# Optimization experiments

Hardware: AMD Instinct MI355X
Metric: run time of the kernel (lower is better)

Reference implementation:

```python
import jax, jax.numpy as jnp
import numpy as np

B, L, D = 16, 1024, 1024
H = 8
K = D // H
OUT = 64

def setup_inputs() -> dict:
    key = jax.random.key(0)
    ks = jax.random.split(key, 12)
    std = 0.1
    return {
        "x0": jax.random.normal(ks[0], (B, L, D), jnp.float32),
        "x1": jax.random.normal(ks[1], (B, L, D), jnp.float32),
        "x2": jax.random.normal(ks[2], (B, L, D), jnp.float32),
        "support": jax.random.normal(ks[3], (B, L), jnp.float32),
        "mask": jnp.ones((B, L), jnp.float32),
        "Wk": std * jax.random.normal(ks[4], (D, D), jnp.float32),   # tokeys.weight
        "Wq": std * jax.random.normal(ks[5], (D, D), jnp.float32),   # toqueries.weight
        "Wv": std * jax.random.normal(ks[6], (D, D), jnp.float32),   # tovalues.weight
        "Wu": std * jax.random.normal(ks[7], (D, D), jnp.float32),   # unifyheads.weight
        "bu": std * jax.random.normal(ks[8], (D,), jnp.float32),     # unifyheads.bias
        "Wmlp": std * jax.random.normal(ks[9], (OUT, D), jnp.float32),
        "bmlp": std * jax.random.normal(ks[10], (OUT,), jnp.float32),
    }

def reference(x0, x1, x2, support, mask, Wk, Wq, Wv, Wu, bu, Wmlp, bmlp):
    # SelfAttention with first=True: q from x2 via tokeys, k from x1 via toqueries, v from x0 via tovalues
    b, l, d = x0.shape
    h, k = H, K
    scale = k ** (-0.25)  # applied to both q and k, as in the torch code
    q = (x2 @ Wk.T).reshape(b, l, h, k) * scale
    key_ = (x1 @ Wq.T).reshape(b, l, h, k) * scale
    v = (x0 @ Wv.T).reshape(b, l, h, k)
    dot = jnp.einsum('blhk,bmhk->bhlm', q, key_)          # [b,h,l,l]
    attn = jax.nn.softmax(dot, axis=-1)
    out = jnp.einsum('bhlm,bmhk->blhk', attn, v).reshape(b, l, d)
    out = out @ Wu.T + bu                                  # unifyheads
    pooled = jnp.mean(out, axis=1) + jnp.max(out, axis=1)  # 'mean_and_max'
    logits = pooled @ Wmlp.T + bmlp                        # dropout = identity (eval)
    return logits
```

## Files before the change

kernel.cpp:

```cpp
#include <hip/hip_runtime.h>

using u16 = unsigned short;
using u32 = unsigned int;
using short8 = __attribute__((ext_vector_type(8))) short;
using floatx4 = __attribute__((ext_vector_type(4))) float;
using floatx16 = __attribute__((ext_vector_type(16))) float;
using u32x4 = __attribute__((ext_vector_type(4))) u32;

__device__ __forceinline__ u32 fbits(float f) { union { float f; u32 u; } v; v.f = f; return v.u; }
__device__ __forceinline__ float fofb(u32 u) { union { u32 u; float f; } v; v.u = u; return v.f; }

__device__ __forceinline__ u16 f2bf(float f) {
    u32 u = fbits(f);
    return (u16)((u + 0x7FFFu + ((u >> 16) & 1u)) >> 16);
}

__device__ __forceinline__ u32 cvtpk_bf16(float lo, float hi) {
    u32 r;
    asm("v_cvt_pk_bf16_f32 %0, %1, %2" : "=v"(r) : "v"(lo), "v"(hi));
    return r;
}

__device__ __forceinline__ void cvt_split8(const float* x, short8& h, short8& l) {
#pragma unroll
    for (int j = 0; j < 8; ++j) {
        u32 b = fbits(x[j]);
        h[j] = (short)(b >> 16);
        float r = x[j] - fofb(b & 0xffff0000u);
        l[j] = (short)(fbits(r) >> 16);
    }
}
__device__ __forceinline__ void cvt_rne8(const float* x, short8& h) {
#pragma unroll
    for (int j = 0; j < 8; ++j) h[j] = (short)f2bf(x[j]);
}

__device__ __forceinline__ void load_lds16(const void* g, u16* l) {
    __builtin_amdgcn_global_load_lds(
        (const __attribute__((address_space(1))) unsigned int*)(g),
        (__attribute__((address_space(3))) unsigned int*)(l), 16, 0, 0);
}

__global__ void convw_kernel(const float* __restrict__ W0, const float* __restrict__ W1,
                             const float* __restrict__ W2, const float* __restrict__ W3,
                             u16* __restrict__ D0, u16* __restrict__ D1,
                             u16* __restrict__ D2, u16* __restrict__ D3) {
    int y = blockIdx.y;
    const float* s = (y == 0) ? W0 : (y == 1) ? W1 : (y == 2) ? W2 : W3;
    u16* d = (y == 0) ? D0 : (y == 1) ? D1 : (y == 2) ? D2 : D3;
    int i = (blockIdx.x * 256 + threadIdx.x) * 4;
    float4 v = *reinterpret_cast<const float4*>(s + i);
    ushort4 h;
    h.x = f2bf(v.x); h.y = f2bf(v.y); h.z = f2bf(v.z); h.w = f2bf(v.w);
    *reinterpret_cast<ushort4*>(d + i) = h;
}

#define GK 1024
#define GN 1024

template<bool SPLIT, bool TRANS, bool POOL, bool FP32A>
__global__ __launch_bounds__(256)
void gemm_bt(const void* __restrict__ Av, const u16* __restrict__ Bh,
             u16* __restrict__ Cb, float scale, u16* __restrict__ Vt,
             float* __restrict__ psum, float* __restrict__ pmax)
{
    constexpr int SM = TRANS ? 17408 : (FP32A ? 12288 : 8192);
    __shared__ __align__(16) u16 smem[SM];

    const int tid  = threadIdx.x;
    const int lane = tid & 63, wave = tid >> 6;
    const int quad = lane >> 4, l15 = lane & 15;
    const int wr = wave >> 1, wc = wave & 1;
    const int bm = blockIdx.x * 128, bn = blockIdx.y * 128;

    const int BOff = FP32A ? 8192 : 4096;

    floatx4 acc[4][4];
#pragma unroll
    for (int mt = 0; mt < 4; ++mt)
#pragma unroll
        for (int nt = 0; nt < 4; ++nt)
#pragma unroll
            for (int r = 0; r < 4; ++r) acc[mt][nt][r] = 0.f;

    const int s8 = (quad ^ ((l15 >> 1) & 3)) * 8;

    for (int kt = 0; kt < GK; kt += 32) {
        __syncthreads();
        if (FP32A) {
            const float* Af = (const float*)Av;
            const int arow = lane >> 3, achk = (lane & 7) ^ (lane >> 3);
            const int brow = lane >> 2, bchk = (lane & 3) ^ ((lane >> 3) & 3);
#pragma unroll
            for (int j = 0; j < 6; ++j) {
                int n = wave + 4 * j;
                if (n < 16) {
                    load_lds16(Af + (size_t)(bm + n * 8 + arow) * GK + kt + achk * 4,
                               smem + n * 512);
                } else {
                    int m = n - 16;
                    load_lds16(Bh + (size_t)(bn + m * 16 + brow) * GK + kt + bchk * 8,
                               smem + 8192 + m * 512);
                }
            }
        } else {
            const u16* Ab = (const u16*)Av;
            const int cgl = (lane & 3) ^ ((lane >> 3) & 3);
            const int rl  = lane >> 2;
            const u16* gp = (wave < 2) ? Ab : Bh;
            int rowb = (wave < 2) ? bm : bn;
            u16* lp = smem + (wave >> 1) * 4096;
            int q0 = (wave & 1) * 4;
#pragma unroll
            for (int q = 0; q < 4; ++q) {
                int qq = q0 + q;
                load_lds16(gp + (size_t)(rowb + qq * 16 + rl) * GK + cgl * 8 + kt,
                           lp + qq * 512);
            }
        }
        __syncthreads();

        short8 a_h[4], a_l[4], b_h[4];
        if (FP32A) {
            const float* Af4 = (const float*)smem;
#pragma unroll
            for (int mt = 0; mt < 4; ++mt) {
                int ra = wr * 64 + mt * 16 + l15;
                int f = ra & 7;
                float xv[8];
                *reinterpret_cast<float4*>(xv) =
                    *reinterpret_cast<const float4*>(Af4 + ra * 32 + (((2 * quad) ^ f) * 4));
                *reinterpret_cast<float4*>(xv + 4) =
                    *reinterpret_cast<const float4*>(Af4 + ra * 32 + (((2 * quad + 1) ^ f) * 4));
                if (SPLIT) cvt_split8(xv, a_h[mt], a_l[mt]);
                else       cvt_rne8(xv, a_h[mt]);
            }
        } else {
#pragma unroll
            for (int mt = 0; mt < 4; ++mt) {
                int ra = wr * 64 + mt * 16 + l15;
                a_h[mt] = *reinterpret_cast<const short8*>(smem + ra * 32 + s8);
            }
        }
#pragma unroll
        for (int nt = 0; nt < 4; ++nt) {
            int rb = wc * 64 + nt * 16 + l15;
            b_h[nt] = *reinterpret_cast<const short8*>(smem + BOff + rb * 32 + s8);
        }
#pragma unroll
        for (int mt = 0; mt < 4; ++mt)
#pragma unroll
            for (int nt = 0; nt < 4; ++nt)
                acc[mt][nt] = __builtin_amdgcn_mfma_f32_16x16x32_bf16(a_h[mt], b_h[nt], acc[mt][nt], 0, 0, 0);
        if (SPLIT) {
#pragma unroll
            for (int mt = 0; mt < 4; ++mt)
#pragma unroll
                for (int nt = 0; nt < 4; ++nt)
                    acc[mt][nt] = __builtin_amdgcn_mfma_f32_16x16x32_bf16(a_l[mt], b_h[nt], acc[mt][nt], 0, 0, 0);
        }
    }

    if (POOL) {
#pragma unroll
        for (int nt = 0; nt < 4; ++nt) {
            float s = 0.f, m = -3.0e38f;
#pragma unroll
            for (int mt = 0; mt < 4; ++mt)
#pragma unroll
                for (int r = 0; r < 4; ++r) {
                    float v = acc[mt][nt][r];
                    s += v; m = fmaxf(m, v);
                }
            s += __shfl_xor(s, 16); s += __shfl_xor(s, 32);
            m = fmaxf(m, __shfl_xor(m, 16)); m = fmaxf(m, __shfl_xor(m, 32));
            if (quad == 0) {
                int col = bn + wc * 64 + nt * 16 + l15;
                int chunk = (bm >> 6) + wr;
                psum[chunk * 1024 + col] = s;
                pmax[chunk * 1024 + col] = m;
            }
        }
    } else if (!TRANS) {
#pragma unroll
        for (int mt = 0; mt < 4; ++mt)
#pragma unroll
            for (int nt = 0; nt < 4; ++nt)
#pragma unroll
                for (int r = 0; r < 4; ++r) {
                    int row = bm + wr * 64 + mt * 16 + quad * 4 + r;
                    int col = bn + wc * 64 + nt * 16 + l15;
                    Cb[(size_t)row * GN + col] = f2bf(acc[mt][nt][r] * scale);
                }
    } else {
        __syncthreads();
#pragma unroll
        for (int mt = 0; mt < 4; ++mt)
#pragma unroll
            for (int nt = 0; nt < 4; ++nt)
#pragma unroll
                for (int r = 0; r < 4; ++r) {
                    int row_local = wr * 64 + mt * 16 + quad * 4 + r;
                    int col_local = wc * 64 + nt * 16 + l15;
                    smem[col_local * 136 + row_local] = f2bf(acc[mt][nt][r]);
                }
        __syncthreads();
        int b = bm >> 10, l0 = bm & 1023, h = bn >> 7;
        int d = tid >> 1, rblk = (tid & 1) * 64;
        u16* gv = Vt + ((size_t)(b * 8 + h) * 128 + d) * 1024 + l0 + rblk;
#pragma unroll
        for (int v = 0; v < 8; ++v)
            *reinterpret_cast<short8*>(gv + v * 8) =
                *reinterpret_cast<const short8*>(smem + d * 136 + rblk + v * 8);
    }
}

#define LOG2E 1.44269504088896f
#define EXPC  46.1662413084470f

__global__ __launch_bounds__(256, 2)
void attn_kernel(const u16* __restrict__ Q, const u16* __restrict__ Kk,
                 const u16* __restrict__ Vt, u16* __restrict__ AO)
{
    __shared__ __align__(16) u16 Ks[2][64 * 128];
    __shared__ __align__(16) u16 Vts[2][128 * 64];

    const int tid  = threadIdx.x;
    const int lane = tid & 63, wave = tid >> 6;
    const int l31 = lane & 31, h2 = lane >> 5;
    const int l7 = lane & 7;

    const int lin = blockIdx.x + (blockIdx.y << 3) + (blockIdx.z << 6);
    const int qt = lin >> 7;
    const int hd = lin & 7;
    const int b  = (lin >> 3) & 15;

    short8 qf[8];
    {
        int qrow = b * 1024 + qt * 128 + wave * 32 + l31;
        const u16* qp = Q + (size_t)qrow * 1024 + hd * 128 + h2 * 8;
#pragma unroll
        for (int s = 0; s < 8; ++s)
            qf[s] = *reinterpret_cast<const short8*>(qp + s * 16);
    }

    float lsum = 0.f;
    floatx16 oacc[4];
#pragma unroll
    for (int db = 0; db < 4; ++db)
#pragma unroll
        for (int r = 0; r < 16; ++r) oacc[db][r] = 0.f;

    const int krow_l = lane >> 4;
    const u16* kgB[4];
#pragma unroll
    for (int i = 0; i < 4; ++i) {
        int cg = (lane & 15) ^ ((i * 4 + krow_l) & 7);
        kgB[i] = Kk + (size_t)(b * 1024 + wave * 16 + i * 4 + krow_l) * 1024
                    + hd * 128 + cg * 8;
    }
    const u16* vtb = Vt + (size_t)(b * 8 + hd) * 128 * 1024;
    const int vrow_l = lane >> 3;
    const u16* vgB = vtb + (size_t)(wave * 32 + vrow_l) * 1024
                         + (((lane & 7) ^ vrow_l) * 8);

#pragma unroll
    for (int i = 0; i < 4; ++i)
        load_lds16(kgB[i], &Ks[0][(wave * 16 + i * 4) * 128]);
#pragma unroll
    for (int i = 0; i < 4; ++i)
        load_lds16(vgB + (size_t)i * 8 * 1024, &Vts[0][(wave * 32 + i * 8) * 64]);

    for (int t = 0; t < 16; ++t) {
        const int cur = t & 1;
        asm volatile("s_waitcnt vmcnt(0)" ::: "memory");
        __builtin_amdgcn_s_barrier();
        __builtin_amdgcn_sched_barrier(0);
        if (t < 15) {
            const int nxt = cur ^ 1;
#pragma unroll
            for (int i = 0; i < 4; ++i)
                load_lds16(kgB[i] + (size_t)(t + 1) * 64 * 1024,
                           &Ks[nxt][(wave * 16 + i * 4) * 128]);
#pragma unroll
            for (int i = 0; i < 4; ++i)
                load_lds16(vgB + (size_t)i * 8 * 1024 + (size_t)(t + 1) * 64,
                           &Vts[nxt][(wave * 32 + i * 8) * 64]);
        }
        const u16* ksb = Ks[cur];
        const u16* vsb = Vts[cur];

        short8 pfr[4];
#pragma unroll
        for (int kb = 0; kb < 2; ++kb) {
            floatx16 sacc;
#pragma unroll
            for (int r = 0; r < 16; ++r) sacc[r] = 0.f;
            __builtin_amdgcn_s_setprio(1);
#pragma unroll
            for (int s = 0; s < 8; ++s) {
                short8 kfr = *reinterpret_cast<const short8*>(
                    &ksb[(kb * 32 + l31) * 128 + (((s * 2 + h2) ^ l7) * 8)]);
                sacc = __builtin_amdgcn_mfma_f32_32x32x16_bf16(kfr, qf[s], sacc, 0, 0, 0);
            }
            __builtin_amdgcn_s_setprio(0);
#pragma unroll
            for (int r = 0; r < 16; ++r) {
                float p = exp2f(fmaf(sacc[r], LOG2E, -EXPC));
                sacc[r] = p;
                lsum += p;
            }
            u32 c0[4], c1[4];
#pragma unroll
            for (int qd = 0; qd < 4; ++qd) {
                c0[qd] = cvtpk_bf16(sacc[4 * qd + 0], sacc[4 * qd + 1]);
                c1[qd] = cvtpk_bf16(sacc[4 * qd + 2], sacc[4 * qd + 3]);
            }
#pragma unroll
            for (int pb = 0; pb < 2; ++pb) {
                auto r1a = __builtin_amdgcn_permlane32_swap(c0[2 * pb],     c1[2 * pb],     false, false);
                auto r2a = __builtin_amdgcn_permlane32_swap(c1[2 * pb],     c0[2 * pb],     false, false);
                auto r1b = __builtin_amdgcn_permlane32_swap(c0[2 * pb + 1], c1[2 * pb + 1], false, false);
                auto r2b = __builtin_amdgcn_permlane32_swap(c1[2 * pb + 1], c0[2 * pb + 1], false, false);
                u32 w0 = h2 ? (u32)r2b[0] : (u32)r1a[0];
                u32 w1 = h2 ? (u32)r1b[0] : (u32)r2a[0];
                u32 w2 = h2 ? (u32)r2b[1] : (u32)r1a[1];
                u32 w3 = h2 ? (u32)r1b[1] : (u32)r2a[1];
                u32x4 ww = {w0, w1, w2, w3};
                pfr[kb * 2 + pb] = __builtin_bit_cast(short8, ww);
            }
        }

        __builtin_amdgcn_s_setprio(1);
#pragma unroll
        for (int ks = 0; ks < 4; ++ks) {
#pragma unroll
            for (int db = 0; db < 4; ++db) {
                int d = db * 32 + l31;
                short8 vfr = *reinterpret_cast<const short8*>(
                    &vsb[d * 64 + (((ks * 2 + h2) ^ l7) * 8)]);
                oacc[db] = __builtin_amdgcn_mfma_f32_32x32x16_bf16(pfr[ks], vfr, oacc[db], 0, 0, 0);
            }
        }
        __builtin_amdgcn_s_setprio(0);
    }

    lsum += __shfl_xor(lsum, 32);

    int qbase = b * 1024 + qt * 128 + wave * 32;
#pragma unroll
    for (int rg = 0; rg < 4; ++rg)
#pragma unroll
        for (int r = 0; r < 4; ++r) {
            int row = rg * 8 + 4 * h2 + r;
            float inv = 1.0f / __shfl(lsum, row);
            u16* ao = AO + (size_t)(qbase + row) * 1024 + hd * 128 + l31;
#pragma unroll
            for (int db = 0; db < 4; ++db)
                ao[db * 32] = f2bf(oacc[db][rg * 4 + r] * inv);
        }
}

__global__ __launch_bounds__(256)
void head_kernel(const float* __restrict__ psum, const float* __restrict__ pmax,
                 const float* __restrict__ bu, const float* __restrict__ Wmlp,
                 const float* __restrict__ bmlp, float* __restrict__ out) {
    __shared__ float pool_s[1024];
    int b = blockIdx.x, tid = threadIdx.x;
    int c4 = tid * 4;
    float4 s = {0.f, 0.f, 0.f, 0.f};
    float4 m = {-3.0e38f, -3.0e38f, -3.0e38f, -3.0e38f};
#pragma unroll
    for (int c = 0; c < 16; ++c) {
        float4 a = *reinterpret_cast<const float4*>(psum + (size_t)(b * 16 + c) * 1024 + c4);
        float4 x = *reinterpret_cast<const float4*>(pmax + (size_t)(b * 16 + c) * 1024 + c4);
        s.x += a.x; s.y += a.y; s.z += a.z; s.w += a.w;
        m.x = fmaxf(m.x, x.x); m.y = fmaxf(m.y, x.y);
        m.z = fmaxf(m.z, x.z); m.w = fmaxf(m.w, x.w);
    }
    float4 bb = *reinterpret_cast<const float4*>(bu + c4);
    pool_s[c4 + 0] = s.x * (1.0f / 1024.0f) + m.x + 2.0f * bb.x;
    pool_s[c4 + 1] = s.y * (1.0f / 1024.0f) + m.y + 2.0f * bb.y;
    pool_s[c4 + 2] = s.z * (1.0f / 1024.0f) + m.z + 2.0f * bb.z;
    pool_s[c4 + 3] = s.w * (1.0f / 1024.0f) + m.w + 2.0f * bb.w;
    __syncthreads();
    int o = tid >> 2, seg = tid & 3;
    const float4* wr = reinterpret_cast<const float4*>(Wmlp + o * 1024 + seg * 256);
    const float4* pr = reinterpret_cast<const float4*>(pool_s + seg * 256);
    float acc = 0.f;
#pragma unroll 8
    for (int i = 0; i < 64; ++i) {
        float4 a = pr[i], w = wr[i];
        acc += a.x * w.x + a.y * w.y + a.z * w.z + a.w * w.w;
    }
    acc += __shfl_xor(acc, 1);
    acc += __shfl_xor(acc, 2);
    if (seg == 0) out[b * 64 + o] = acc + bmlp[o];
}

extern "C" void kernel_launch(void* const* d_in, const int* in_sizes, int n_in,
                              void* d_out, int out_size, void* d_ws, size_t ws_size,
                              hipStream_t stream) {
    const float* x0 = (const float*)d_in[0];
    const float* x1 = (const float*)d_in[1];
    const float* x2 = (const float*)d_in[2];
    const float* Wk = (const float*)d_in[5];
    const float* Wq = (const float*)d_in[6];
    const float* Wv = (const float*)d_in[7];
    const float* Wu = (const float*)d_in[8];
    const float* bu = (const float*)d_in[9];
    const float* Wmlp = (const float*)d_in[10];
    const float* bmlp = (const float*)d_in[11];
    float* out = (float*)d_out;

    char* ws = (char*)d_ws;
    const size_t MB32 = 33554432ull;
    size_t wo = 0;
    u16* Wkh = (u16*)(ws + wo); wo += 2097152;
    u16* Wqh = (u16*)(ws + wo); wo += 2097152;
    u16* Wvh = (u16*)(ws + wo); wo += 2097152;
    u16* Wuh = (u16*)(ws + wo); wo += 2097152;
    u16* Qb = (u16*)(ws + wo); wo += MB32;
    u16* Kb = (u16*)(ws + wo); wo += MB32;
    u16* Vt = (u16*)(ws + wo); wo += MB32;
    u16* AOb = (u16*)(ws + wo); wo += MB32;
    float* psum = (float*)(ws + wo); wo += 1048576;
    float* pmax = (float*)(ws + wo); wo += 1048576;
    if (ws_size < wo) return;

    const float scale = 0.29730177875068026f;

    convw_kernel<<<dim3(1024, 4), 256, 0, stream>>>(Wk, Wq, Wv, Wu, Wkh, Wqh, Wvh, Wuh);

    dim3 ggrid(128, 8);
    gemm_bt<true, false, false, true><<<ggrid, 256, 0, stream>>>(x2, Wkh, Qb, scale, nullptr, nullptr, nullptr);
    gemm_bt<true, false, false, true><<<ggrid, 256, 0, stream>>>(x1, Wqh, Kb, scale, nullptr, nullptr, nullptr);
    gemm_bt<false, true, false, true><<<ggrid, 256, 0, stream>>>(x0, Wvh, nullptr, 1.0f, Vt, nullptr, nullptr);

    dim3 agrid(8, 8, 16);
    attn_kernel<<<agrid, 256, 0, stream>>>(Qb, Kb, Vt, AOb);

    gemm_bt<false, false, true, false><<<ggrid, 256, 0, stream>>>(AOb, Wuh, nullptr, 1.0f, nullptr, psum, pmax);

    head_kernel<<<16, 256, 0, stream>>>(psum, pmax, bu, Wmlp, bmlp, out);
}
```

Measured before the change: 596.4 us.

## Pre-split fp32 activations into bf16 hi/lo and run K=2048 bf16 GEMMs

Adds a conversion pass that writes each fp32 input as concatenated bf16 hi and lo halves, and duplicates Wk/Wq along K. The Q/K projections then become plain bf16 GEMMs with K=2048 instead of fp32-A loads with in-kernel split conversion, and the V projection uses a pre-rounded bf16 input. The intent is to remove the fp32 LDS traffic and the per-tile conversion work inside the GEMM. The cost is three extra elementwise passes over 64MB inputs, extra workspace traffic, and a doubled K loop for two GEMMs.

```diff
diff --git a/kernel.cpp b/kernel.cpp
--- a/kernel.cpp
+++ b/kernel.cpp
@@ -41,6 +41,7 @@
         (__attribute__((address_space(3))) unsigned int*)(l), 16, 0, 0);
 }
 
+template<bool DUP>
 __global__ void convw_kernel(const float* __restrict__ W0, const float* __restrict__ W1,
                              const float* __restrict__ W2, const float* __restrict__ W3,
                              u16* __restrict__ D0, u16* __restrict__ D1,
@@ -52,13 +53,47 @@
     float4 v = *reinterpret_cast<const float4*>(s + i);
     ushort4 h;
     h.x = f2bf(v.x); h.y = f2bf(v.y); h.z = f2bf(v.z); h.w = f2bf(v.w);
-    *reinterpret_cast<ushort4*>(d + i) = h;
-}
-
-#define GK 1024
+    if (DUP && y < 2) {
+        int n = i >> 10, k = i & 1023;
+        u16* base = d + (size_t)n * 2048 + k;
+        *reinterpret_cast<ushort4*>(base) = h;
+        *reinterpret_cast<ushort4*>(base + 1024) = h;
+    } else {
+        *reinterpret_cast<ushort4*>(d + i) = h;
+    }
+}
+
+template<bool SPLIT>
+__global__ __launch_bounds__(256)
+void convx_kernel(const float* __restrict__ X, u16* __restrict__ O) {
+    int i = (blockIdx.x * 256 + threadIdx.x) * 4;
+    float4 v = *reinterpret_cast<const float4*>(X + i);
+    if (SPLIT) {
+        int m = i >> 10, k = i & 1023;
+        float xs[4] = {v.x, v.y, v.z, v.w};
+        ushort4 h, l;
+        u16 hh[4], ll[4];
+#pragma unroll
+        for (int j = 0; j < 4; ++j) {
+            u32 b = fbits(xs[j]);
+            hh[j] = (u16)(b >> 16);
+            float r = xs[j] - fofb(b & 0xffff0000u);
+            ll[j] = (u16)(fbits(r) >> 16);
+        }
+        h.x = hh[0]; h.y = hh[1]; h.z = hh[2]; h.w = hh[3];
+        l.x = ll[0]; l.y = ll[1]; l.z = ll[2]; l.w = ll[3];
+        *reinterpret_cast<ushort4*>(O + (size_t)m * 2048 + k) = h;
+        *reinterpret_cast<ushort4*>(O + (size_t)m * 2048 + 1024 + k) = l;
+    } else {
+        ushort4 h;
+        h.x = f2bf(v.x); h.y = f2bf(v.y); h.z = f2bf(v.z); h.w = f2bf(v.w);
+        *reinterpret_cast<ushort4*>(O + i) = h;
+    }
+}
+
 #define GN 1024
 
-template<bool SPLIT, bool TRANS, bool POOL, bool FP32A>
+template<int KDIM, bool SPLIT, bool TRANS, bool POOL, bool FP32A>
 __global__ __launch_bounds__(256)
 void gemm_bt(const void* __restrict__ Av, const u16* __restrict__ Bh,
              u16* __restrict__ Cb, float scale, u16* __restrict__ Vt,
@@ -85,7 +120,7 @@
 
     const int s8 = (quad ^ ((l15 >> 1) & 3)) * 8;
 
-    for (int kt = 0; kt < GK; kt += 32) {
+    for (int kt = 0; kt < KDIM; kt += 32) {
         __syncthreads();
         if (FP32A) {
             const float* Af = (const float*)Av;
@@ -95,11 +130,11 @@
             for (int j = 0; j < 6; ++j) {
                 int n = wave + 4 * j;
                 if (n < 16) {
-                    load_lds16(Af + (size_t)(bm + n * 8 + arow) * GK + kt + achk * 4,
+                    load_lds16(Af + (size_t)(bm + n * 8 + arow) * KDIM + kt + achk * 4,
                                smem + n * 512);
                 } else {
                     int m = n - 16;
-                    load_lds16(Bh + (size_t)(bn + m * 16 + brow) * GK + kt + bchk * 8,
+                    load_lds16(Bh + (size_t)(bn + m * 16 + brow) * KDIM + kt + bchk * 8,
                                smem + 8192 + m * 512);
                 }
             }
@@ -114,7 +149,7 @@
 #pragma unroll
             for (int q = 0; q < 4; ++q) {
                 int qq = q0 + q;
-                load_lds16(gp + (size_t)(rowb + qq * 16 + rl) * GK + cgl * 8 + kt,
+                load_lds16(gp + (size_t)(rowb + qq * 16 + rl) * KDIM + cgl * 8 + kt,
                            lp + qq * 512);
             }
         }
@@ -414,6 +449,43 @@
     float* out = (float*)d_out;
 
     char* ws = (char*)d_ws;
+    const size_t MB = 1048576ull;
+    const float scale = 0.29730177875068026f;
+
+    const size_t wo_new = 4 * MB + 4 * MB + 2 * MB + 2 * MB + 64 * MB + 32 * MB + 32 * MB;
+    if (ws_size >= wo_new) {
+        u16* Wk2 = (u16*)(ws);
+        u16* Wq2 = (u16*)(ws + 4 * MB);
+        u16* Wvh = (u16*)(ws + 8 * MB);
+        u16* Wuh = (u16*)(ws + 10 * MB);
+        u16* XS  = (u16*)(ws + 12 * MB);
+        u16* Qb  = (u16*)(ws + 76 * MB);
+        u16* Kb  = (u16*)(ws + 108 * MB);
+        u16* Vt  = XS + 16 * MB;
+        u16* AOb = XS;
+        float* psum = (float*)Qb;
+        float* pmax = (float*)((char*)Qb + 1 * MB);
+
+        convw_kernel<true><<<dim3(1024, 4), 256, 0, stream>>>(Wk, Wq, Wv, Wu, Wk2, Wq2, Wvh, Wuh);
+
+        dim3 ggrid(128, 8);
+
+        convx_kernel<true><<<16384, 256, 0, stream>>>(x2, XS);
+        gemm_bt<2048, false, false, false, false><<<ggrid, 256, 0, stream>>>(XS, Wk2, Qb, scale, nullptr, nullptr, nullptr);
+        convx_kernel<true><<<16384, 256, 0, stream>>>(x1, XS);
+        gemm_bt<2048, false, false, false, false><<<ggrid, 256, 0, stream>>>(XS, Wq2, Kb, scale, nullptr, nullptr, nullptr);
+        convx_kernel<false><<<16384, 256, 0, stream>>>(x0, XS);
+        gemm_bt<1024, false, true, false, false><<<ggrid, 256, 0, stream>>>(XS, Wvh, nullptr, 1.0f, Vt, nullptr, nullptr);
+
+        dim3 agrid(8, 8, 16);
+        attn_kernel<<<agrid, 256, 0, stream>>>(Qb, Kb, Vt, AOb);
+
+        gemm_bt<1024, false, false, true, false><<<ggrid, 256, 0, stream>>>(AOb, Wuh, nullptr, 1.0f, nullptr, psum, pmax);
+
+        head_kernel<<<16, 256, 0, stream>>>(psum, pmax, bu, Wmlp, bmlp, out);
+        return;
+    }
+
     const size_t MB32 = 33554432ull;
     size_t wo = 0;
     u16* Wkh = (u16*)(ws + wo); wo += 2097152;
@@ -428,19 +500,17 @@
     float* pmax = (float*)(ws + wo); wo += 1048576;
     if (ws_size < wo) return;
 
-    const float scale = 0.29730177875068026f;
-
-    convw_kernel<<<dim3(1024, 4), 256, 0, stream>>>(Wk, Wq, Wv, Wu, Wkh, Wqh, Wvh, Wuh);
+    convw_kernel<false><<<dim3(1024, 4), 256, 0, stream>>>(Wk, Wq, Wv, Wu, Wkh, Wqh, Wvh, Wuh);
 
     dim3 ggrid(128, 8);
-    gemm_bt<true, false, false, true><<<ggrid, 256, 0, stream>>>(x2, Wkh, Qb, scale, nullptr, nullptr, nullptr);
-    gemm_bt<true, false, false, true><<<ggrid, 256, 0, stream>>>(x1, Wqh, Kb, scale, nullptr, nullptr, nullptr);
-    gemm_bt<false, true, false, true><<<ggrid, 256, 0, stream>>>(x0, Wvh, nullptr, 1.0f, Vt, nullptr, nullptr);
+    gemm_bt<1024, true, false, false, true><<<ggrid, 256, 0, stream>>>(x2, Wkh, Qb, scale, nullptr, nullptr, nullptr);
+    gemm_bt<1024, true, false, false, true><<<ggrid, 256, 0, stream>>>(x1, Wqh, Kb, scale, nullptr, nullptr, nullptr);
+    gemm_bt<1024, false, true, false, true><<<ggrid, 256, 0, stream>>>(x0, Wvh, nullptr, 1.0f, Vt, nullptr, nullptr);
 
     dim3 agrid(8, 8, 16);
     attn_kernel<<<agrid, 256, 0, stream>>>(Qb, Kb, Vt, AOb);
 
-    gemm_bt<false, false, true, false><<<ggrid, 256, 0, stream>>>(AOb, Wuh, nullptr, 1.0f, nullptr, psum, pmax);
+    gemm_bt<1024, false, false, true, false><<<ggrid, 256, 0, stream>>>(AOb, Wuh, nullptr, 1.0f, nullptr, psum, pmax);
 
     head_kernel<<<16, 256, 0, stream>>>(psum, pmax, bu, Wmlp, bmlp, out);
 }
```

Result: slower. 629.2 us (+5.5%).
